# Performance work log

Hardware: AMD Instinct MI355X
Metric: run time of the kernel (lower is better)

Reference implementation:

```python
import jax, jax.numpy as jnp
import numpy as np

B, N, DIN, DOUT, E, K = 64, 883, 2, 64, 10, 2
CIN = DIN + DOUT


def _dgcn(x, node_emb, time, day, speed, occupy,
          fc1_w, fc1_b, fc2_w, fc2_b, fc3_w, fc3_b, wpool, bpool):
    # x: (B, N, C); node_emb: (N, E); time/day/speed/occupy: (B, N, E)
    n = x.shape[1]
    # hyper-network filter from input features
    h = jax.nn.sigmoid(x @ fc1_w + fc1_b)
    h = jax.nn.sigmoid(h @ fc2_w + fc2_b)
    filt = h @ fc3_w + fc3_b                                  # (B, N, E)
    # dynamic node embedding: static emb modulated by time/day/speed/occupy embeddings
    dyn = node_emb[None] * time * day * speed * occupy        # (B, N, E)
    nodevec = jnp.tanh(dyn * filt)                            # (B, N, E)
    A = jax.nn.relu(jnp.einsum('bne,bme->bnm', nodevec, nodevec))  # (B, N, N)
    d = jnp.sum(A, axis=-1) ** -0.5                           # (B, N)
    I = jnp.eye(n, dtype=x.dtype)
    L = I[None] - A * d[:, :, None] * d[:, None, :]           # normalized laplacian support
    # cheb_k = 2 supports: identity and L
    x_g = jnp.stack([x, jnp.einsum('bnm,bmc->bnc', L, x)], axis=2)  # (B, N, K, C)
    weights = jnp.einsum('ne,ekio->nkio', node_emb, wpool)    # (N, K, C, O)
    bias = node_emb @ bpool                                   # (N, O)
    return jnp.einsum('bnki,nkio->bno', x_g, weights) + bias[None]


def setup_inputs() -> dict:
    key = jax.random.key(0)
    ks = jax.random.split(key, 23)
    rn = lambda k, s, sc=1.0: jax.random.normal(k, s, dtype=jnp.float32) * sc
    return dict(
        x=rn(ks[0], (B, N, DIN)),
        state=rn(ks[1], (B, N, DOUT), 0.1),
        node_embeddings=rn(ks[2], (N, E)),
        time=rn(ks[3], (B, N, E), 0.5),
        day=rn(ks[4], (B, N, E), 0.5),
        speed=rn(ks[5], (B, N, E), 0.5),
        occupy=rn(ks[6], (B, N, E), 0.5),
        gate_wpool=rn(ks[7], (E, K, CIN, 2 * DOUT), 0.1),
        gate_bpool=rn(ks[8], (E, 2 * DOUT), 0.1),
        gate_fc1_w=rn(ks[9], (CIN, 16), 0.1), gate_fc1_b=rn(ks[10], (16,), 0.1),
        gate_fc2_w=rn(ks[11], (16, 2), 0.1), gate_fc2_b=rn(ks[12], (2,), 0.1),
        gate_fc3_w=rn(ks[13], (2, E), 0.1), gate_fc3_b=rn(ks[14], (E,), 0.1),
        update_wpool=rn(ks[15], (E, K, CIN, DOUT), 0.1),
        update_bpool=rn(ks[16], (E, DOUT), 0.1),
        update_fc1_w=rn(ks[17], (CIN, 16), 0.1), update_fc1_b=rn(ks[18], (16,), 0.1),
        update_fc2_w=rn(ks[19], (16, 2), 0.1), update_fc2_b=rn(ks[20], (2,), 0.1),
        update_fc3_w=rn(ks[21], (2, E), 0.1), update_fc3_b=rn(ks[22], (E,), 0.1),
    )


def reference(x, state, node_embeddings, time, day, speed, occupy,
              gate_wpool, gate_bpool, gate_fc1_w, gate_fc1_b, gate_fc2_w,
              gate_fc2_b, gate_fc3_w, gate_fc3_b,
              update_wpool, update_bpool, update_fc1_w, update_fc1_b,
              update_fc2_w, update_fc2_b, update_fc3_w, update_fc3_b):
    xs = jnp.concatenate([x, state], axis=-1)                 # (B, N, DIN+DOUT)
    z_r = jax.nn.sigmoid(_dgcn(xs, node_embeddings, time, day, speed, occupy,
                               gate_fc1_w, gate_fc1_b, gate_fc2_w, gate_fc2_b,
                               gate_fc3_w, gate_fc3_b, gate_wpool, gate_bpool))
    z, r = jnp.split(z_r, 2, axis=-1)
    cand = jnp.concatenate([x, z * state], axis=-1)
    hc = jnp.tanh(_dgcn(cand, node_embeddings, time, day, speed, occupy,
                        update_fc1_w, update_fc1_b, update_fc2_w, update_fc2_b,
                        update_fc3_w, update_fc3_b, update_wpool, update_bpool))
    return r * state + (1.0 - r) * hc
```

## Files before the change

kernel.cpp:

```cpp
#include <hip/hip_runtime.h>
#include <cmath>

#define BB 64
#define NN 883
#define NP 896
#define EE 10
#define CC 66
#define KP 160

typedef __attribute__((ext_vector_type(8))) short bf16x8;
typedef __attribute__((ext_vector_type(4))) float f32x4;

__device__ __forceinline__ float sigmoidf_(float v) { return 1.f / (1.f + expf(-v)); }

__device__ __forceinline__ unsigned short f2bf(float f) {
  unsigned int u = __float_as_uint(f);
  u = u + 0x7FFFu + ((u >> 16) & 1u);
  return (unsigned short)(u >> 16);
}
__device__ __forceinline__ float bf2f(unsigned short h) {
  return __uint_as_float(((unsigned int)h) << 16);
}

template<int PHASE>
__global__ __launch_bounds__(256) void k1_hyper(
    const float* __restrict__ x, const float* __restrict__ state,
    const float* __restrict__ zr, const float* __restrict__ emb,
    const float* __restrict__ tme, const float* __restrict__ day,
    const float* __restrict__ spd, const float* __restrict__ occ,
    const float* __restrict__ w1, const float* __restrict__ b1,
    const float* __restrict__ w2, const float* __restrict__ b2,
    const float* __restrict__ w3, const float* __restrict__ b3,
    unsigned short* __restrict__ Acat, unsigned short* __restrict__ nvP) {
  int idx = blockIdx.x * 256 + threadIdx.x;
  if (idx >= BB * NP) return;
  int b = idx / NP, n = idx - b * NP;
  if (n >= NN) {
    *(uint4*)&nvP[(size_t)idx * 16] = make_uint4(0, 0, 0, 0);
    *(uint4*)&nvP[(size_t)idx * 16 + 8] = make_uint4(0, 0, 0, 0);
    return;
  }
  int bn = b * NN + n;

  float xsr[CC];
  xsr[0] = x[bn * 2 + 0];
  xsr[1] = x[bn * 2 + 1];
#pragma unroll
  for (int j = 0; j < 64; ++j) {
    float s = state[bn * 64 + j];
    if (PHASE == 1) s *= zr[(size_t)bn * 128 + j];
    xsr[2 + j] = s;
  }
  {
    unsigned short a16[80];
#pragma unroll
    for (int c = 0; c < CC; ++c) a16[c] = f2bf(xsr[c]);
#pragma unroll
    for (int c = CC; c < 80; ++c) a16[c] = 0;
#pragma unroll
    for (int k = 0; k < 10; ++k) {
      unsigned int w0 = (unsigned int)a16[8 * k + 0] | ((unsigned int)a16[8 * k + 1] << 16);
      unsigned int w1 = (unsigned int)a16[8 * k + 2] | ((unsigned int)a16[8 * k + 3] << 16);
      unsigned int w2_ = (unsigned int)a16[8 * k + 4] | ((unsigned int)a16[8 * k + 5] << 16);
      unsigned int w3_ = (unsigned int)a16[8 * k + 6] | ((unsigned int)a16[8 * k + 7] << 16);
      *(uint4*)&Acat[(size_t)bn * KP + 8 * k] = make_uint4(w0, w1, w2_, w3_);
    }
  }

  float h1[16];
#pragma unroll
  for (int j = 0; j < 16; ++j) h1[j] = b1[j];
#pragma unroll
  for (int i = 0; i < CC; ++i) {
    float xv = xsr[i];
#pragma unroll
    for (int j = 0; j < 16; ++j) h1[j] = fmaf(xv, w1[i * 16 + j], h1[j]);
  }
#pragma unroll
  for (int j = 0; j < 16; ++j) h1[j] = sigmoidf_(h1[j]);

  float h2[2];
#pragma unroll
  for (int j = 0; j < 2; ++j) {
    float s = b2[j];
#pragma unroll
    for (int i = 0; i < 16; ++i) s = fmaf(h1[i], w2[i * 2 + j], s);
    h2[j] = sigmoidf_(s);
  }

  unsigned short nv16[16];
#pragma unroll
  for (int e = 0; e < EE; ++e) {
    float f = b3[e] + h2[0] * w3[e] + h2[1] * w3[EE + e];
    int be = bn * EE + e;
    float dyn = emb[n * EE + e] * tme[be] * day[be] * spd[be] * occ[be];
    nv16[e] = f2bf(tanhf(dyn * f));
  }
#pragma unroll
  for (int e = EE; e < 16; ++e) nv16[e] = 0;
  unsigned int w[8];
#pragma unroll
  for (int k = 0; k < 8; ++k)
    w[k] = (unsigned int)nv16[2 * k] | ((unsigned int)nv16[2 * k + 1] << 16);
  *(uint4*)&nvP[(size_t)idx * 16]     = make_uint4(w[0], w[1], w[2], w[3]);
  *(uint4*)&nvP[(size_t)idx * 16 + 8] = make_uint4(w[4], w[5], w[6], w[7]);
}

__global__ __launch_bounds__(256) void k2_deg(const unsigned short* __restrict__ nvP,
                                              float* __restrict__ dd) {
  int nt = blockIdx.x, b = blockIdx.y;
  int t = threadIdx.x, wid = t >> 6, lane = t & 63;
  int col = lane & 15, q = lane >> 4;
  int n16 = nt * 64 + wid * 16;

  bf16x8 anv = {0, 0, 0, 0, 0, 0, 0, 0};
  if (q < 2) anv = *(const bf16x8*)&nvP[((size_t)(b * NP + n16 + col)) * 16 + q * 8];

  float rs0 = 0.f, rs1 = 0.f, rs2 = 0.f, rs3 = 0.f;
  for (int mb = 0; mb < NP; mb += 16) {
    bf16x8 bfr = {0, 0, 0, 0, 0, 0, 0, 0};
    if (q < 2) bfr = *(const bf16x8*)&nvP[((size_t)(b * NP + mb + col)) * 16 + q * 8];
    f32x4 z = {0.f, 0.f, 0.f, 0.f};
    f32x4 g = __builtin_amdgcn_mfma_f32_16x16x32_bf16(anv, bfr, z, 0, 0, 0);
    rs0 += fmaxf(g[0], 0.f);
    rs1 += fmaxf(g[1], 0.f);
    rs2 += fmaxf(g[2], 0.f);
    rs3 += fmaxf(g[3], 0.f);
  }
#pragma unroll
  for (int off = 1; off < 16; off <<= 1) {
    rs0 += __shfl_xor(rs0, off);
    rs1 += __shfl_xor(rs1, off);
    rs2 += __shfl_xor(rs2, off);
    rs3 += __shfl_xor(rs3, off);
  }
  if (col == 0) {
    int base = b * NP + n16 + q * 4;
    dd[base + 0] = rs0;
    dd[base + 1] = rs1;
    dd[base + 2] = rs2;
    dd[base + 3] = rs3;
  }
}

__global__ __launch_bounds__(256) void k2b_xsd(const float* __restrict__ dd,
                                               const unsigned short* __restrict__ Acat,
                                               float* __restrict__ d_g,
                                               unsigned short* __restrict__ xsdT) {
  int mt = blockIdx.x, b = blockIdx.y, t = threadIdx.x;
  __shared__ float tile[64][67];
  __shared__ float d_s[64];
  int mb = mt * 64;
  if (t < 64) {
    int m = mb + t;
    float dv = 0.f;
    if (m < NN) dv = rsqrtf(dd[b * NP + m]);
    d_s[t] = dv;
    d_g[b * NP + m] = dv;
  }
  for (int idx = t; idx < 64 * CC; idx += 256) {
    int ml = idx / CC, c = idx - ml * CC;
    int m = mb + ml;
    float v = 0.f;
    if (m < NN) v = bf2f(Acat[((size_t)(b * NN + m)) * KP + c]);
    tile[ml][c] = v;
  }
  __syncthreads();
  for (int idx = t; idx < CC * 64; idx += 256) {
    int c = idx >> 6, ml = idx & 63;
    xsdT[((size_t)(b * CC) + c) * NP + mb + ml] = f2bf(tile[ml][c] * d_s[ml]);
  }
}

__global__ __launch_bounds__(256) void k3_agg(const unsigned short* __restrict__ nvP,
                                              const float* __restrict__ d_g,
                                              const unsigned short* __restrict__ xsdT,
                                              unsigned short* __restrict__ Acat) {
  int nt = blockIdx.x, b = blockIdx.y, t = threadIdx.x;
  int wid = t >> 6, lane = t & 63, col = lane & 15, q = lane >> 4;
  int n16 = nt * 64 + wid * 16;
  __shared__ __align__(16) unsigned short As[4][16 * 40];
  unsigned short* wAs = As[wid];

  bf16x8 anv = {0, 0, 0, 0, 0, 0, 0, 0};
  if (q < 2) anv = *(const bf16x8*)&nvP[((size_t)(b * NP + n16 + col)) * 16 + q * 8];

  f32x4 acc[5];
#pragma unroll
  for (int ct = 0; ct < 5; ++ct) acc[ct] = (f32x4){0.f, 0.f, 0.f, 0.f};

  for (int mb = 0; mb < NP; mb += 32) {
    bf16x8 b0 = {0, 0, 0, 0, 0, 0, 0, 0};
    bf16x8 b1 = {0, 0, 0, 0, 0, 0, 0, 0};
    if (q < 2) {
      b0 = *(const bf16x8*)&nvP[((size_t)(b * NP + mb + col)) * 16 + q * 8];
      b1 = *(const bf16x8*)&nvP[((size_t)(b * NP + mb + 16 + col)) * 16 + q * 8];
    }
    f32x4 z = {0.f, 0.f, 0.f, 0.f};
    f32x4 g0 = __builtin_amdgcn_mfma_f32_16x16x32_bf16(anv, b0, z, 0, 0, 0);
    f32x4 g1 = __builtin_amdgcn_mfma_f32_16x16x32_bf16(anv, b1, z, 0, 0, 0);
#pragma unroll
    for (int r = 0; r < 4; ++r) {
      wAs[(q * 4 + r) * 40 + col]      = f2bf(fmaxf(g0[r], 0.f));
      wAs[(q * 4 + r) * 40 + col + 16] = f2bf(fmaxf(g1[r], 0.f));
    }
    bf16x8 afr = *(const bf16x8*)&wAs[col * 40 + q * 8];
#pragma unroll
    for (int ct = 0; ct < 5; ++ct) {
      int c = ct * 16 + col;
      bf16x8 xf = {0, 0, 0, 0, 0, 0, 0, 0};
      if (c < CC) xf = *(const bf16x8*)&xsdT[((size_t)(b * CC) + c) * NP + mb + q * 8];
      acc[ct] = __builtin_amdgcn_mfma_f32_16x16x32_bf16(afr, xf, acc[ct], 0, 0, 0);
    }
  }

  float dn[4];
#pragma unroll
  for (int r = 0; r < 4; ++r) dn[r] = d_g[b * NP + n16 + q * 4 + r];
#pragma unroll
  for (int ct = 0; ct < 5; ++ct) {
    int c = ct * 16 + col;
#pragma unroll
    for (int r = 0; r < 4; ++r) {
      int n = n16 + q * 4 + r;
      if (n < NN)
        Acat[((size_t)(b * NN) + n) * KP + 80 + c] = f2bf(-(acc[ct][r] * dn[r]));
    }
  }
}

template<int OT, bool GATE>
__global__ __launch_bounds__(256) void k4b_gemm(
    const float* __restrict__ emb, const float* __restrict__ wpool,
    const float* __restrict__ bpool, const unsigned short* __restrict__ Acat,
    float* __restrict__ zr_w,
    const float* __restrict__ state, const float* __restrict__ zr_r,
    float* __restrict__ out) {
  int n = blockIdx.x, t = threadIdx.x;
  __shared__ __align__(16) unsigned short Ws[OT * 168];
  __shared__ float bias_s[OT];

  const int OG = OT / 4;
  int og = t % OG, ti = t / OG;
  int o4 = og * 4;
  float em[EE];
#pragma unroll
  for (int e = 0; e < EE; ++e) em[e] = emb[n * EE + e];

  for (int i = ti; i < CC; i += 256 / OG) {
    float4 s0 = make_float4(0.f, 0.f, 0.f, 0.f);
    float4 s1 = make_float4(0.f, 0.f, 0.f, 0.f);
#pragma unroll
    for (int e = 0; e < EE; ++e) {
      float4 w0 = *(const float4*)&wpool[(((size_t)(e * 2 + 0) * CC + i)) * OT + o4];
      float4 w1 = *(const float4*)&wpool[(((size_t)(e * 2 + 1) * CC + i)) * OT + o4];
      s0.x = fmaf(em[e], w0.x, s0.x); s0.y = fmaf(em[e], w0.y, s0.y);
      s0.z = fmaf(em[e], w0.z, s0.z); s0.w = fmaf(em[e], w0.w, s0.w);
      s1.x = fmaf(em[e], w1.x, s1.x); s1.y = fmaf(em[e], w1.y, s1.y);
      s1.z = fmaf(em[e], w1.z, s1.z); s1.w = fmaf(em[e], w1.w, s1.w);
    }
    Ws[(o4 + 0) * 168 + i] = f2bf(s0.x + s1.x);
    Ws[(o4 + 1) * 168 + i] = f2bf(s0.y + s1.y);
    Ws[(o4 + 2) * 168 + i] = f2bf(s0.z + s1.z);
    Ws[(o4 + 3) * 168 + i] = f2bf(s0.w + s1.w);
    Ws[(o4 + 0) * 168 + 80 + i] = f2bf(s1.x);
    Ws[(o4 + 1) * 168 + 80 + i] = f2bf(s1.y);
    Ws[(o4 + 2) * 168 + 80 + i] = f2bf(s1.z);
    Ws[(o4 + 3) * 168 + 80 + i] = f2bf(s1.w);
  }
  for (int idx = t; idx < OT * 14; idx += 256) {
    int o = idx / 14, kk = idx - o * 14;
    Ws[o * 168 + 66 + kk] = 0;
    Ws[o * 168 + 146 + kk] = 0;
  }
  if (t < OT) {
    float s = 0.f;
#pragma unroll
    for (int e = 0; e < EE; ++e) s = fmaf(em[e] * 0.f + emb[n * EE + e], bpool[e * OT + t], s);
    bias_s[t] = s;
  }
  __syncthreads();

  int wid = t >> 6, lane = t & 63, col = lane & 15, q = lane >> 4;
  int bA = wid * 16 + col;
  f32x4 acc[OT / 16];
#pragma unroll
  for (int ot = 0; ot < OT / 16; ++ot) acc[ot] = (f32x4){0.f, 0.f, 0.f, 0.f};

#pragma unroll
  for (int ks = 0; ks < 5; ++ks) {
    bf16x8 af = *(const bf16x8*)&Acat[((size_t)(bA * NN + n)) * KP + ks * 32 + q * 8];
#pragma unroll
    for (int ot = 0; ot < OT / 16; ++ot) {
      bf16x8 bf = *(const bf16x8*)&Ws[(ot * 16 + col) * 168 + ks * 32 + q * 8];
      acc[ot] = __builtin_amdgcn_mfma_f32_16x16x32_bf16(af, bf, acc[ot], 0, 0, 0);
    }
  }

#pragma unroll
  for (int ot = 0; ot < OT / 16; ++ot) {
    int o = ot * 16 + col;
    float bia = bias_s[o];
#pragma unroll
    for (int r = 0; r < 4; ++r) {
      int bb = wid * 16 + q * 4 + r;
      float v = acc[ot][r] + bia;
      if (GATE) {
        zr_w[((size_t)(bb * NN + n)) * 128 + o] = sigmoidf_(v);
      } else {
        float hc = tanhf(v);
        float rr = zr_r[((size_t)(bb * NN + n)) * 128 + 64 + o];
        float st = state[((size_t)(bb * NN + n)) * 64 + o];
        out[((size_t)(bb * NN + n)) * 64 + o] = fmaf(rr, st - hc, hc);
      }
    }
  }
}

extern "C" void kernel_launch(void* const* d_in, const int* in_sizes, int n_in,
                              void* d_out, int out_size, void* d_ws, size_t ws_size,
                              hipStream_t stream) {
  const float* x     = (const float*)d_in[0];
  const float* state = (const float*)d_in[1];
  const float* emb   = (const float*)d_in[2];
  const float* tme   = (const float*)d_in[3];
  const float* day   = (const float*)d_in[4];
  const float* spd   = (const float*)d_in[5];
  const float* occ   = (const float*)d_in[6];
  const float* gwp   = (const float*)d_in[7];
  const float* gbp   = (const float*)d_in[8];
  const float* gw1   = (const float*)d_in[9];
  const float* gb1   = (const float*)d_in[10];
  const float* gw2   = (const float*)d_in[11];
  const float* gb2   = (const float*)d_in[12];
  const float* gw3   = (const float*)d_in[13];
  const float* gb3   = (const float*)d_in[14];
  const float* uwp   = (const float*)d_in[15];
  const float* ubp   = (const float*)d_in[16];
  const float* uw1   = (const float*)d_in[17];
  const float* ub1   = (const float*)d_in[18];
  const float* uw2   = (const float*)d_in[19];
  const float* ub2   = (const float*)d_in[20];
  const float* uw3   = (const float*)d_in[21];
  const float* ub3   = (const float*)d_in[22];

  char* w = (char*)d_ws;
  unsigned short* Acat = (unsigned short*)w;  w += (size_t)BB * NN * KP * 2;
  unsigned short* nvP  = (unsigned short*)w;  w += (size_t)BB * NP * 16 * 2;
  unsigned short* xsdT = (unsigned short*)w;  w += (size_t)BB * CC * NP * 2;
  float* dd   = (float*)w;  w += (size_t)BB * NP * 4;
  float* d_g  = (float*)w;  w += (size_t)BB * NP * 4;
  float* zr   = (float*)w;  w += (size_t)BB * NN * 128 * 4;

  dim3 b256(256);
  dim3 gK1((BB * NP) / 256);
  dim3 gK2(14, BB);
  dim3 gK4(NN);

  k1_hyper<0><<<gK1, b256, 0, stream>>>(x, state, zr, emb, tme, day, spd, occ,
                                        gw1, gb1, gw2, gb2, gw3, gb3, Acat, nvP);
  k2_deg<<<gK2, b256, 0, stream>>>(nvP, dd);
  k2b_xsd<<<gK2, b256, 0, stream>>>(dd, Acat, d_g, xsdT);
  k3_agg<<<gK2, b256, 0, stream>>>(nvP, d_g, xsdT, Acat);
  k4b_gemm<128, true><<<gK4, b256, 0, stream>>>(emb, gwp, gbp, Acat, zr,
                                                nullptr, nullptr, nullptr);
  k1_hyper<1><<<gK1, b256, 0, stream>>>(x, state, zr, emb, tme, day, spd, occ,
                                        uw1, ub1, uw2, ub2, uw3, ub3, Acat, nvP);
  k2_deg<<<gK2, b256, 0, stream>>>(nvP, dd);
  k2b_xsd<<<gK2, b256, 0, stream>>>(dd, Acat, d_g, xsdT);
  k3_agg<<<gK2, b256, 0, stream>>>(nvP, d_g, xsdT, Acat);
  k4b_gemm<64, false><<<gK4, b256, 0, stream>>>(emb, uwp, ubp, Acat, nullptr,
                                                state, zr, (float*)d_out);
}
```

Baseline: 426.0 us.

## Fuse degree and scaled-x kernels, software-pipeline aggregation with double-buffered LDS

Merges the degree computation and the degree-scaled transposed-x kernel into one launch, since each block's 64 nodes match the rows it scales. This removes the dd buffer round trip and one launch per DGCN. The aggregation kernel is restructured into a software pipeline: it prefetches the next nodevec and x fragments, swaps MFMA operand order so results pack straight into transposed LDS stores, and double-buffers the LDS tile so the second MFMA stage uses the previous tile. It also drops a dummy term from the bias computation. The cost is extra registers for prefetched fragments, which may lower occupancy.

New measurement: 435.4 us. 2.2% more time.

```diff
diff --git a/kernel.cpp b/kernel.cpp
--- a/kernel.cpp
+++ b/kernel.cpp
@@ -107,68 +107,61 @@
 }
 
 __global__ __launch_bounds__(256) void k2_deg(const unsigned short* __restrict__ nvP,
-                                              float* __restrict__ dd) {
+                                              const unsigned short* __restrict__ Acat,
+                                              float* __restrict__ d_g,
+                                              unsigned short* __restrict__ xsdT) {
   int nt = blockIdx.x, b = blockIdx.y;
   int t = threadIdx.x, wid = t >> 6, lane = t & 63;
   int col = lane & 15, q = lane >> 4;
   int n16 = nt * 64 + wid * 16;
-
-  bf16x8 anv = {0, 0, 0, 0, 0, 0, 0, 0};
-  if (q < 2) anv = *(const bf16x8*)&nvP[((size_t)(b * NP + n16 + col)) * 16 + q * 8];
-
-  float rs0 = 0.f, rs1 = 0.f, rs2 = 0.f, rs3 = 0.f;
-  for (int mb = 0; mb < NP; mb += 16) {
-    bf16x8 bfr = {0, 0, 0, 0, 0, 0, 0, 0};
-    if (q < 2) bfr = *(const bf16x8*)&nvP[((size_t)(b * NP + mb + col)) * 16 + q * 8];
-    f32x4 z = {0.f, 0.f, 0.f, 0.f};
-    f32x4 g = __builtin_amdgcn_mfma_f32_16x16x32_bf16(anv, bfr, z, 0, 0, 0);
-    rs0 += fmaxf(g[0], 0.f);
-    rs1 += fmaxf(g[1], 0.f);
-    rs2 += fmaxf(g[2], 0.f);
-    rs3 += fmaxf(g[3], 0.f);
-  }
-#pragma unroll
-  for (int off = 1; off < 16; off <<= 1) {
-    rs0 += __shfl_xor(rs0, off);
-    rs1 += __shfl_xor(rs1, off);
-    rs2 += __shfl_xor(rs2, off);
-    rs3 += __shfl_xor(rs3, off);
-  }
-  if (col == 0) {
-    int base = b * NP + n16 + q * 4;
-    dd[base + 0] = rs0;
-    dd[base + 1] = rs1;
-    dd[base + 2] = rs2;
-    dd[base + 3] = rs3;
-  }
-}
-
-__global__ __launch_bounds__(256) void k2b_xsd(const float* __restrict__ dd,
-                                               const unsigned short* __restrict__ Acat,
-                                               float* __restrict__ d_g,
-                                               unsigned short* __restrict__ xsdT) {
-  int mt = blockIdx.x, b = blockIdx.y, t = threadIdx.x;
   __shared__ float tile[64][67];
   __shared__ float d_s[64];
-  int mb = mt * 64;
-  if (t < 64) {
-    int m = mb + t;
-    float dv = 0.f;
-    if (m < NN) dv = rsqrtf(dd[b * NP + m]);
-    d_s[t] = dv;
-    d_g[b * NP + m] = dv;
-  }
+
+  const unsigned short* nvb = nvP + (size_t)b * NP * 16;
+  bf16x8 zf = {0, 0, 0, 0, 0, 0, 0, 0};
+  bf16x8 anv = zf;
+  if (q < 2) anv = *(const bf16x8*)&nvb[(size_t)(n16 + col) * 16 + q * 8];
+
+  float rs[4] = {0.f, 0.f, 0.f, 0.f};
+  bf16x8 cur = zf, nxt = zf;
+  if (q < 2) cur = *(const bf16x8*)&nvb[(size_t)col * 16 + q * 8];
+  for (int mb = 0; mb < NP; mb += 16) {
+    if (q < 2 && mb + 16 < NP)
+      nxt = *(const bf16x8*)&nvb[(size_t)(mb + 16 + col) * 16 + q * 8];
+    f32x4 z = {0.f, 0.f, 0.f, 0.f};
+    f32x4 g = __builtin_amdgcn_mfma_f32_16x16x32_bf16(anv, cur, z, 0, 0, 0);
+#pragma unroll
+    for (int r = 0; r < 4; ++r) rs[r] += fmaxf(g[r], 0.f);
+    cur = nxt;
+  }
+#pragma unroll
+  for (int off = 1; off < 16; off <<= 1) {
+#pragma unroll
+    for (int r = 0; r < 4; ++r) rs[r] += __shfl_xor(rs[r], off);
+  }
+  if (col == 0) {
+#pragma unroll
+    for (int r = 0; r < 4; ++r) {
+      int n = n16 + q * 4 + r;
+      float dv = (n < NN) ? rsqrtf(rs[r]) : 0.f;
+      d_g[b * NP + n] = dv;
+      d_s[wid * 16 + q * 4 + r] = dv;
+    }
+  }
+  __syncthreads();
+
+  int mb = nt * 64;
   for (int idx = t; idx < 64 * CC; idx += 256) {
     int ml = idx / CC, c = idx - ml * CC;
     int m = mb + ml;
     float v = 0.f;
     if (m < NN) v = bf2f(Acat[((size_t)(b * NN + m)) * KP + c]);
-    tile[ml][c] = v;
+    tile[ml][c] = v * d_s[ml];
   }
   __syncthreads();
   for (int idx = t; idx < CC * 64; idx += 256) {
     int c = idx >> 6, ml = idx & 63;
-    xsdT[((size_t)(b * CC) + c) * NP + mb + ml] = f2bf(tile[ml][c] * d_s[ml]);
+    xsdT[((size_t)(b * CC) + c) * NP + mb + ml] = f2bf(tile[ml][c]);
   }
 }
 
@@ -179,39 +172,91 @@
   int nt = blockIdx.x, b = blockIdx.y, t = threadIdx.x;
   int wid = t >> 6, lane = t & 63, col = lane & 15, q = lane >> 4;
   int n16 = nt * 64 + wid * 16;
-  __shared__ __align__(16) unsigned short As[4][16 * 40];
-  unsigned short* wAs = As[wid];
-
-  bf16x8 anv = {0, 0, 0, 0, 0, 0, 0, 0};
-  if (q < 2) anv = *(const bf16x8*)&nvP[((size_t)(b * NP + n16 + col)) * 16 + q * 8];
+  __shared__ __align__(16) unsigned short As[4][2][16 * 40];
+  unsigned short* wAs0 = As[wid][0];
+  unsigned short* wAs1 = As[wid][1];
+
+  const unsigned short* nvb = nvP + (size_t)b * NP * 16;
+  const unsigned short* xb = xsdT + (size_t)b * CC * NP;
+
+  bf16x8 zf = {0, 0, 0, 0, 0, 0, 0, 0};
+  bf16x8 anv = zf;
+  if (q < 2) anv = *(const bf16x8*)&nvb[(size_t)(n16 + col) * 16 + q * 8];
 
   f32x4 acc[5];
 #pragma unroll
   for (int ct = 0; ct < 5; ++ct) acc[ct] = (f32x4){0.f, 0.f, 0.f, 0.f};
 
-  for (int mb = 0; mb < NP; mb += 32) {
-    bf16x8 b0 = {0, 0, 0, 0, 0, 0, 0, 0};
-    bf16x8 b1 = {0, 0, 0, 0, 0, 0, 0, 0};
+  int cg[5];
+  bool cok[5];
+#pragma unroll
+  for (int ct = 0; ct < 5; ++ct) { cg[ct] = ct * 16 + col; cok[ct] = cg[ct] < CC; }
+
+  bf16x8 nv0 = zf, nv1 = zf, nv0n = zf, nv1n = zf;
+  bf16x8 xs2[5], xsn[5];
+
+  if (q < 2) {
+    nv0 = *(const bf16x8*)&nvb[(size_t)(0 + col) * 16 + q * 8];
+    nv1 = *(const bf16x8*)&nvb[(size_t)(16 + col) * 16 + q * 8];
+  }
+
+  {
     if (q < 2) {
-      b0 = *(const bf16x8*)&nvP[((size_t)(b * NP + mb + col)) * 16 + q * 8];
-      b1 = *(const bf16x8*)&nvP[((size_t)(b * NP + mb + 16 + col)) * 16 + q * 8];
-    }
+      nv0n = *(const bf16x8*)&nvb[(size_t)(32 + col) * 16 + q * 8];
+      nv1n = *(const bf16x8*)&nvb[(size_t)(48 + col) * 16 + q * 8];
+    }
+#pragma unroll
+    for (int ct = 0; ct < 5; ++ct)
+      xsn[ct] = cok[ct] ? *(const bf16x8*)&xb[(size_t)cg[ct] * NP + 0 + q * 8] : zf;
     f32x4 z = {0.f, 0.f, 0.f, 0.f};
-    f32x4 g0 = __builtin_amdgcn_mfma_f32_16x16x32_bf16(anv, b0, z, 0, 0, 0);
-    f32x4 g1 = __builtin_amdgcn_mfma_f32_16x16x32_bf16(anv, b1, z, 0, 0, 0);
-#pragma unroll
-    for (int r = 0; r < 4; ++r) {
-      wAs[(q * 4 + r) * 40 + col]      = f2bf(fmaxf(g0[r], 0.f));
-      wAs[(q * 4 + r) * 40 + col + 16] = f2bf(fmaxf(g1[r], 0.f));
-    }
-    bf16x8 afr = *(const bf16x8*)&wAs[col * 40 + q * 8];
-#pragma unroll
-    for (int ct = 0; ct < 5; ++ct) {
-      int c = ct * 16 + col;
-      bf16x8 xf = {0, 0, 0, 0, 0, 0, 0, 0};
-      if (c < CC) xf = *(const bf16x8*)&xsdT[((size_t)(b * CC) + c) * NP + mb + q * 8];
-      acc[ct] = __builtin_amdgcn_mfma_f32_16x16x32_bf16(afr, xf, acc[ct], 0, 0, 0);
-    }
+    f32x4 g0 = __builtin_amdgcn_mfma_f32_16x16x32_bf16(nv0, anv, z, 0, 0, 0);
+    f32x4 g1 = __builtin_amdgcn_mfma_f32_16x16x32_bf16(nv1, anv, z, 0, 0, 0);
+    unsigned int a0 = (unsigned int)f2bf(fmaxf(g0[0], 0.f)) | ((unsigned int)f2bf(fmaxf(g0[1], 0.f)) << 16);
+    unsigned int a1 = (unsigned int)f2bf(fmaxf(g0[2], 0.f)) | ((unsigned int)f2bf(fmaxf(g0[3], 0.f)) << 16);
+    unsigned int b0 = (unsigned int)f2bf(fmaxf(g1[0], 0.f)) | ((unsigned int)f2bf(fmaxf(g1[1], 0.f)) << 16);
+    unsigned int b1 = (unsigned int)f2bf(fmaxf(g1[2], 0.f)) | ((unsigned int)f2bf(fmaxf(g1[3], 0.f)) << 16);
+    *(uint2*)&wAs0[col * 40 + 0 + q * 4] = make_uint2(a0, a1);
+    *(uint2*)&wAs0[col * 40 + 16 + q * 4] = make_uint2(b0, b1);
+    nv0 = nv0n; nv1 = nv1n;
+#pragma unroll
+    for (int ct = 0; ct < 5; ++ct) xs2[ct] = xsn[ct];
+  }
+
+  for (int i = 1; i < 28; ++i) {
+    unsigned short* curB = (i & 1) ? wAs1 : wAs0;
+    unsigned short* prvB = (i & 1) ? wAs0 : wAs1;
+    bf16x8 afr = *(const bf16x8*)&prvB[col * 40 + q * 8];
+    int mbn = (i + 1) * 32;
+    if (i < 27 && q < 2) {
+      nv0n = *(const bf16x8*)&nvb[(size_t)(mbn + col) * 16 + q * 8];
+      nv1n = *(const bf16x8*)&nvb[(size_t)(mbn + 16 + col) * 16 + q * 8];
+    }
+    int mb = i * 32;
+#pragma unroll
+    for (int ct = 0; ct < 5; ++ct)
+      xsn[ct] = cok[ct] ? *(const bf16x8*)&xb[(size_t)cg[ct] * NP + mb + q * 8] : zf;
+    f32x4 z = {0.f, 0.f, 0.f, 0.f};
+    f32x4 g0 = __builtin_amdgcn_mfma_f32_16x16x32_bf16(nv0, anv, z, 0, 0, 0);
+    f32x4 g1 = __builtin_amdgcn_mfma_f32_16x16x32_bf16(nv1, anv, z, 0, 0, 0);
+    unsigned int a0 = (unsigned int)f2bf(fmaxf(g0[0], 0.f)) | ((unsigned int)f2bf(fmaxf(g0[1], 0.f)) << 16);
+    unsigned int a1 = (unsigned int)f2bf(fmaxf(g0[2], 0.f)) | ((unsigned int)f2bf(fmaxf(g0[3], 0.f)) << 16);
+    unsigned int b0 = (unsigned int)f2bf(fmaxf(g1[0], 0.f)) | ((unsigned int)f2bf(fmaxf(g1[1], 0.f)) << 16);
+    unsigned int b1 = (unsigned int)f2bf(fmaxf(g1[2], 0.f)) | ((unsigned int)f2bf(fmaxf(g1[3], 0.f)) << 16);
+    *(uint2*)&curB[col * 40 + 0 + q * 4] = make_uint2(a0, a1);
+    *(uint2*)&curB[col * 40 + 16 + q * 4] = make_uint2(b0, b1);
+#pragma unroll
+    for (int ct = 0; ct < 5; ++ct)
+      acc[ct] = __builtin_amdgcn_mfma_f32_16x16x32_bf16(afr, xs2[ct], acc[ct], 0, 0, 0);
+    nv0 = nv0n; nv1 = nv1n;
+#pragma unroll
+    for (int ct = 0; ct < 5; ++ct) xs2[ct] = xsn[ct];
+  }
+
+  {
+    bf16x8 afr = *(const bf16x8*)&wAs1[col * 40 + q * 8];
+#pragma unroll
+    for (int ct = 0; ct < 5; ++ct)
+      acc[ct] = __builtin_amdgcn_mfma_f32_16x16x32_bf16(afr, xs2[ct], acc[ct], 0, 0, 0);
   }
 
   float dn[4];
@@ -276,7 +321,7 @@
   if (t < OT) {
     float s = 0.f;
 #pragma unroll
-    for (int e = 0; e < EE; ++e) s = fmaf(em[e] * 0.f + emb[n * EE + e], bpool[e * OT + t], s);
+    for (int e = 0; e < EE; ++e) s = fmaf(em[e], bpool[e * OT + t], s);
     bias_s[t] = s;
   }
   __syncthreads();
@@ -348,7 +393,6 @@
   unsigned short* Acat = (unsigned short*)w;  w += (size_t)BB * NN * KP * 2;
   unsigned short* nvP  = (unsigned short*)w;  w += (size_t)BB * NP * 16 * 2;
   unsigned short* xsdT = (unsigned short*)w;  w += (size_t)BB * CC * NP * 2;
-  float* dd   = (float*)w;  w += (size_t)BB * NP * 4;
   float* d_g  = (float*)w;  w += (size_t)BB * NP * 4;
   float* zr   = (float*)w;  w += (size_t)BB * NN * 128 * 4;
 
@@ -359,15 +403,13 @@
 
   k1_hyper<0><<<gK1, b256, 0, stream>>>(x, state, zr, emb, tme, day, spd, occ,
                                         gw1, gb1, gw2, gb2, gw3, gb3, Acat, nvP);
-  k2_deg<<<gK2, b256, 0, stream>>>(nvP, dd);
-  k2b_xsd<<<gK2, b256, 0, stream>>>(dd, Acat, d_g, xsdT);
+  k2_deg<<<gK2, b256, 0, stream>>>(nvP, Acat, d_g, xsdT);
   k3_agg<<<gK2, b256, 0, stream>>>(nvP, d_g, xsdT, Acat);
   k4b_gemm<128, true><<<gK4, b256, 0, stream>>>(emb, gwp, gbp, Acat, zr,
                                                 nullptr, nullptr, nullptr);
   k1_hyper<1><<<gK1, b256, 0, stream>>>(x, state, zr, emb, tme, day, spd, occ,
                                         uw1, ub1, uw2, ub2, uw3, ub3, Acat, nvP);
-  k2_deg<<<gK2, b256, 0, stream>>>(nvP, dd);
-  k2b_xsd<<<gK2, b256, 0, stream>>>(dd, Acat, d_g, xsdT);
+  k2_deg<<<gK2, b256, 0, stream>>>(nvP, Acat, d_g, xsdT);
   k3_agg<<<gK2, b256, 0, stream>>>(nvP, d_g, xsdT, Acat);
   k4b_gemm<64, false><<<gK4, b256, 0, stream>>>(emb, uwp, ubp, Acat, nullptr,
                                                 state, zr, (float*)d_out);
```
